# Kernel optimization log

Measured on AMD Instinct MI355X. Metric: run time of the kernel, lower is better.

Reference implementation:

```python
import jax, jax.numpy as jnp
import numpy as np

DIM = 768
EPS = 1e-06


def _layernorm(x, gamma, beta):
    # LayerNorm over last axis (channels), eps=EPS, elementwise affine
    mu = jnp.mean(x, axis=-1, keepdims=True)
    var = jnp.mean(jnp.square(x - mu), axis=-1, keepdims=True)
    return (x - mu) * jax.lax.rsqrt(var + EPS) * gamma + beta


def setup_inputs() -> dict:
    key = jax.random.key(0)
    ks = jax.random.split(key, 10)
    B, C, H, W = 16, DIM, 32, 32
    s = 1.0 / np.sqrt(C)  # mimic Conv2d default init scale
    return {
        "x": jax.random.normal(ks[0], (B, C, H, W), dtype=jnp.float32),
        "W1": jax.random.uniform(ks[1], (C, C), jnp.float32, -s, s),
        "b1": jax.random.uniform(ks[2], (C,), jnp.float32, -s, s),
        "g1": jnp.ones((C,), jnp.float32),
        "beta1": jnp.zeros((C,), jnp.float32),
        "W2": jax.random.uniform(ks[3], (C, C), jnp.float32, -s, s),
        "b2": jax.random.uniform(ks[4], (C,), jnp.float32, -s, s),
        "g2": jnp.ones((C,), jnp.float32),
        "beta2": jnp.zeros((C,), jnp.float32),
        "W3": jax.random.uniform(ks[5], (C, C), jnp.float32, -s, s),
        "b3": jax.random.uniform(ks[6], (C,), jnp.float32, -s, s),
    }


def reference(x, W1, b1, g1, beta1, W2, b2, g2, beta2, W3, b3):
    # x: [B, C, H, W] (NCHW). Work in NHWC; 1x1 conv == channel matmul.
    h = jnp.transpose(x, (0, 2, 3, 1))  # [B, H, W, C]
    h = jnp.einsum("bhwc,oc->bhwo", h, W1) + b1
    h = jax.nn.gelu(_layernorm(h, g1, beta1), approximate=False)
    h = jnp.einsum("bhwc,oc->bhwo", h, W2) + b2
    h = jax.nn.gelu(_layernorm(h, g2, beta2), approximate=False)
    h = jnp.einsum("bhwc,oc->bhwo", h, W3) + b3
    return jnp.transpose(h, (0, 3, 1, 2))  # back to NCHW
```

## Files before the change

kernel.cpp:

```cpp
#include <hip/hip_runtime.h>
#include <hip/hip_bf16.h>

typedef __bf16 bf16;
typedef __bf16 bf16x4 __attribute__((ext_vector_type(4)));
typedef __bf16 bf16x8 __attribute__((ext_vector_type(8)));
typedef float f32x4 __attribute__((ext_vector_type(4)));

#define DIM 768
#define HW 1024
#define BATCH 16
#define M_TOTAL (BATCH * HW)
#define NKT 12

#define AS1 __attribute__((address_space(1)))
#define AS3 __attribute__((address_space(3)))


__global__ void wcvt3_kernel(const float4* __restrict__ w1, const float4* __restrict__ w2,
                             const float4* __restrict__ w3,
                             bf16x8* __restrict__ o1, bf16x8* __restrict__ o2,
                             bf16x8* __restrict__ o3) {
    const int b = blockIdx.x;
    const int which = b / 288;
    const int i = (b % 288) * 256 + threadIdx.x;
    const float4* w = which == 0 ? w1 : which == 1 ? w2 : w3;
    bf16x8* o = which == 0 ? o1 : which == 1 ? o2 : o3;
    const int row = i / 96, br = i % 96;
    const int q = br >> 2, g = br & 3;
    float4 lo = w[row * 192 + q * 8 + g];
    float4 hi = w[row * 192 + q * 8 + g + 4];
    bf16x8 r = { (bf16)lo.x, (bf16)lo.y, (bf16)lo.z, (bf16)lo.w,
                 (bf16)hi.x, (bf16)hi.y, (bf16)hi.z, (bf16)hi.w };
    o[row * 96 + br] = r;
}

__global__ void transpose_cvt_kernel(const float* __restrict__ x, bf16* __restrict__ xb) {
    __shared__ float tile[32][33];
    const int b = blockIdx.z;
    const int hw0 = blockIdx.x * 32;
    const int c0 = blockIdx.y * 32;
    const int tx = threadIdx.x, ty = threadIdx.y;

    const float* src = x + ((size_t)b * DIM + c0) * HW + hw0;
#pragma unroll
    for (int j = 0; j < 4; j++)
        tile[ty + 8 * j][tx] = src[(size_t)(ty + 8 * j) * HW + tx];
    __syncthreads();
    const int ptx = (((tx & 15) >> 2) << 3) + (tx & 3) + ((tx >> 4) << 2);
    bf16* dst = xb + ((size_t)b * HW + hw0) * DIM + c0;
#pragma unroll
    for (int j = 0; j < 4; j++)
        dst[(size_t)(ty + 8 * j) * DIM + ptx] = (bf16)tile[tx][ty + 8 * j];
}

template <int MODE>
__global__ __launch_bounds__(512, 2) void gemm_kernel(
    const bf16* __restrict__ A,
    const bf16* __restrict__ Bw,
    const float* __restrict__ bias,
    void* __restrict__ out)
{
    constexpr int K = DIM;
    __shared__ bf16 ldsA[2][256][64];
    __shared__ bf16 ldsB[2][192][64];

    const int t = threadIdx.x;
    const int lane = t & 63;
    const int wave = t >> 6;
    const int wm = wave >> 1, wn = wave & 1;

    const int bid = blockIdx.x;
    const int swz = (bid & 7) * 32 + (bid >> 3);
    const int m0 = (swz & 63) << 8;
    const int n0 = (swz >> 6) * 192;

    const int fr = lane & 15;
    const int fq = lane >> 4;

    f32x4 acc[4][6] = {};

    const int s_r = t >> 3;
    const int s_blk = t & 7;

    auto stage_chunk = [&](int kt, int which, int chunk) {
        const int d = kt & 1;
        const int r = chunk * 64 + s_r;
        if (which == 0)
            __builtin_amdgcn_global_load_lds(
                (const AS1 void*)(A + (size_t)(m0 + r) * K + kt * 64 + ((s_blk ^ (r & 7)) << 3)),
                (AS3 void*)&ldsA[d][r][s_blk * 8], 16, 0, 0);
        else
            __builtin_amdgcn_global_load_lds(
                (const AS1 void*)(Bw + (size_t)(n0 + r) * K + kt * 64 + ((s_blk ^ (r & 7)) << 3)),
                (AS3 void*)&ldsB[d][r][s_blk * 8], 16, 0, 0);
    };

    bf16x8 a[4], b0[6], b1[6];

    auto ldA = [&](int kt, int mh) {
        const int d = kt & 1;
#pragma unroll
        for (int mi = 0; mi < 2; mi++) {
            const int R = wm * 64 + (mh * 2 + mi) * 16 + fr;
            const bf16* rp = &ldsA[d][R][0];
            const int s = R & 7;
#pragma unroll
            for (int ks = 0; ks < 2; ks++)
                a[mi * 2 + ks] = *(const bf16x8*)(rp + (((ks * 4 + fq) ^ s) << 3));
        }
    };
    auto ldB = [&](bf16x8* bb, int kt, int nh) {
        const int d = kt & 1;
#pragma unroll
        for (int ni = 0; ni < 3; ni++) {
            const int R = wn * 96 + (nh * 3 + ni) * 16 + fr;
            const bf16* rp = &ldsB[d][R][0];
            const int s = R & 7;
#pragma unroll
            for (int ks = 0; ks < 2; ks++)
                bb[ni * 2 + ks] = *(const bf16x8*)(rp + (((ks * 4 + fq) ^ s) << 3));
        }
    };
    auto MM = [&](bf16x8* bb, int mh, int nh) {
        __builtin_amdgcn_s_setprio(1);
#pragma unroll
        for (int mi = 0; mi < 2; mi++)
#pragma unroll
            for (int ni = 0; ni < 3; ni++)
#pragma unroll
                for (int ks = 0; ks < 2; ks++)
                    acc[mh * 2 + mi][nh * 3 + ni] = __builtin_amdgcn_mfma_f32_16x16x32_bf16(
                        a[mi * 2 + ks], bb[ni * 2 + ks], acc[mh * 2 + mi][nh * 3 + ni], 0, 0, 0);
        __builtin_amdgcn_s_setprio(0);
    };

    stage_chunk(0, 0, 0); stage_chunk(0, 0, 1); stage_chunk(0, 0, 2); stage_chunk(0, 0, 3);
    stage_chunk(0, 1, 0); stage_chunk(0, 1, 1); stage_chunk(0, 1, 2);
    stage_chunk(1, 0, 0); stage_chunk(1, 0, 1);
    asm volatile("s_waitcnt vmcnt(2)" ::: "memory");
    __builtin_amdgcn_s_barrier();

    for (int kt = 0; kt < NKT; ++kt) {
        ldA(kt, 0);
        ldB(b0, kt, 0);
        if (kt + 1 < NKT) { stage_chunk(kt + 1, 0, 2); stage_chunk(kt + 1, 0, 3); }
        __builtin_amdgcn_s_barrier();
        asm volatile("s_waitcnt lgkmcnt(0)" ::: "memory");
        MM(b0, 0, 0);
        __builtin_amdgcn_s_barrier();
        ldB(b1, kt, 1);
        if (kt + 1 < NKT) { stage_chunk(kt + 1, 1, 0); stage_chunk(kt + 1, 1, 1); }
        __builtin_amdgcn_s_barrier();
        asm volatile("s_waitcnt lgkmcnt(0)" ::: "memory");
        MM(b1, 0, 1);
        __builtin_amdgcn_s_barrier();
        ldA(kt, 1);
        if (kt + 1 < NKT) stage_chunk(kt + 1, 1, 2);
        __builtin_amdgcn_s_barrier();
        asm volatile("s_waitcnt lgkmcnt(0)" ::: "memory");
        MM(b1, 1, 1);
        __builtin_amdgcn_s_barrier();
        if (kt + 2 < NKT) { stage_chunk(kt + 2, 0, 0); stage_chunk(kt + 2, 0, 1); }
        MM(b0, 1, 0);
        if (kt < NKT - 2) { asm volatile("s_waitcnt vmcnt(2)" ::: "memory"); }
        else if (kt == NKT - 2) { asm volatile("s_waitcnt vmcnt(0)" ::: "memory"); }
        __builtin_amdgcn_s_barrier();
    }

    const int fq4 = fq * 4;
    if (MODE == 0) {
        bf16* o = (bf16*)out;
#pragma unroll
        for (int mi = 0; mi < 4; mi++) {
            const int row = m0 + wm * 64 + mi * 16 + fq4;
#pragma unroll
            for (int ni = 0; ni < 6; ni++) {
                const int col = n0 + wn * 96 + ni * 16 + fr;
                const int pcol = n0 + wn * 96 + ((ni >> 1) << 5)
                               + ((fr >> 2) << 3) + (fr & 3) + ((ni & 1) << 2);
                const float bv = bias[col];
#pragma unroll
                for (int r = 0; r < 4; r++)
                    o[(size_t)(row + r) * DIM + pcol] = (bf16)(acc[mi][ni][r] + bv);
            }
        }
    } else {
        float* o = (float*)out;
#pragma unroll
        for (int mi = 0; mi < 4; mi++) {
            const int nb = m0 + wm * 64 + mi * 16 + fq4;
            const int bI = nb >> 10, hw = nb & 1023;
#pragma unroll
            for (int ni = 0; ni < 6; ni++) {
                const int col = n0 + wn * 96 + ni * 16 + fr;
                f32x4 v = acc[mi][ni] + bias[col];
                *(f32x4*)(o + ((size_t)bI * DIM + col) * HW + hw) = v;
            }
        }
    }
}

__global__ __launch_bounds__(256) void ln_gelu_kernel(
    bf16* __restrict__ h, const float* __restrict__ g, const float* __restrict__ beta)
{
    const int wave = threadIdx.x >> 6;
    const int lane = threadIdx.x & 63;
    const int n = blockIdx.x * 4 + wave;
    bf16* row = h + (size_t)n * DIM;

    float v[12];
    float s = 0.f, ss = 0.f;
#pragma unroll
    for (int j = 0; j < 3; j++) {
        bf16x4 x = *(const bf16x4*)(row + j * 256 + lane * 4);
#pragma unroll
        for (int i = 0; i < 4; i++) {
            float f = (float)x[i];
            v[j * 4 + i] = f;
            s += f;
            ss += f * f;
        }
    }
#pragma unroll
    for (int off = 32; off > 0; off >>= 1) {
        s += __shfl_xor(s, off);
        ss += __shfl_xor(ss, off);
    }
    const float mu = s * (1.f / DIM);
    const float var = ss * (1.f / DIM) - mu * mu;
    const float rstd = rsqrtf(var + 1e-6f);

#pragma unroll
    for (int j = 0; j < 3; j++) {
        bf16x4 r;
#pragma unroll
        for (int i = 0; i < 4; i++) {
            const int c = j * 256 + lane * 4 + i;
            const int p = (lane * 4 + i) & 31;
            const int kk = ((p >> 3) << 2) + (p & 7) + ((p & 4) ? 12 : 0);
            const int gi = (c & ~31) + kk;
            float y = (v[j * 4 + i] - mu) * rstd * g[gi] + beta[gi];
            y = 0.5f * y * (1.f + erff(y * 0.70710678118f));
            r[i] = (bf16)y;
        }
        *(bf16x4*)(row + j * 256 + lane * 4) = r;
    }
}

extern "C" void kernel_launch(void* const* d_in, const int* in_sizes, int n_in,
                              void* d_out, int out_size, void* d_ws, size_t ws_size,
                              hipStream_t stream) {
    const float* x   = (const float*)d_in[0];
    const float* W1  = (const float*)d_in[1];
    const float* b1  = (const float*)d_in[2];
    const float* g1  = (const float*)d_in[3];
    const float* be1 = (const float*)d_in[4];
    const float* W2  = (const float*)d_in[5];
    const float* b2  = (const float*)d_in[6];
    const float* g2  = (const float*)d_in[7];
    const float* be2 = (const float*)d_in[8];
    const float* W3  = (const float*)d_in[9];
    const float* b3  = (const float*)d_in[10];
    float* out = (float*)d_out;

    bf16* Wb1  = (bf16*)d_ws;
    bf16* Wb2  = Wb1 + (size_t)DIM * DIM;
    bf16* Wb3  = Wb2 + (size_t)DIM * DIM;
    bf16* buf0 = Wb3 + (size_t)DIM * DIM;
    bf16* buf1 = buf0 + (size_t)M_TOTAL * DIM;

    wcvt3_kernel<<<864, 256, 0, stream>>>((const float4*)W1, (const float4*)W2, (const float4*)W3,
                                          (bf16x8*)Wb1, (bf16x8*)Wb2, (bf16x8*)Wb3);

    transpose_cvt_kernel<<<dim3(32, 24, 16), dim3(32, 8), 0, stream>>>(x, buf0);

    const int ggrid = (M_TOTAL / 256) * (DIM / 192);
    gemm_kernel<0><<<ggrid, 512, 0, stream>>>(buf0, Wb1, b1, buf1);
    ln_gelu_kernel<<<M_TOTAL / 4, 256, 0, stream>>>(buf1, g1, be1);
    gemm_kernel<0><<<ggrid, 512, 0, stream>>>(buf1, Wb2, b2, buf0);
    ln_gelu_kernel<<<M_TOTAL / 4, 256, 0, stream>>>(buf0, g2, be2);
    gemm_kernel<1><<<ggrid, 512, 0, stream>>>(buf0, Wb3, b3, out);
}
```

Baseline: 161.9 us.

## Fuse LayerNorm+GELU into GEMM epilogue with full-row 64x768 tiles

Restructures each GEMM so a block owns 64 complete output rows across all 768 channels. This lets the LayerNorm statistics be reduced in-block through shared memory and GELU applied in the epilogue, which removes the two standalone ln_gelu kernels and their extra read/write passes over the activations. The K loop now runs in 32-wide steps and streams the whole weight matrix per block through a double-buffered LDS buffer. The grid shrinks to 256 blocks, one per CU, which cuts parallelism and raises per-block weight traffic.

Result: no change. 162.5 us (+0.4%).

```diff
diff --git a/kernel.cpp b/kernel.cpp
--- a/kernel.cpp
+++ b/kernel.cpp
@@ -10,7 +10,7 @@
 #define HW 1024
 #define BATCH 16
 #define M_TOTAL (BATCH * HW)
-#define NKT 12
+#define NKT 24
 
 #define AS1 __attribute__((address_space(1)))
 #define AS3 __attribute__((address_space(3)))
@@ -58,192 +58,179 @@
     const bf16* __restrict__ A,
     const bf16* __restrict__ Bw,
     const float* __restrict__ bias,
+    const float* __restrict__ gamma,
+    const float* __restrict__ beta,
     void* __restrict__ out)
 {
-    constexpr int K = DIM;
-    __shared__ bf16 ldsA[2][256][64];
-    __shared__ bf16 ldsB[2][192][64];
+    __shared__ bf16 ldsB[2][DIM][32];
+    __shared__ bf16 ldsA[2][64][64];
+    __shared__ float lnred[64][4][2];
 
     const int t = threadIdx.x;
     const int lane = t & 63;
     const int wave = t >> 6;
-    const int wm = wave >> 1, wn = wave & 1;
+    const int wm = wave >> 2, wn = wave & 3;
 
     const int bid = blockIdx.x;
     const int swz = (bid & 7) * 32 + (bid >> 3);
-    const int m0 = (swz & 63) << 8;
-    const int n0 = (swz >> 6) * 192;
-
-    const int fr = lane & 15;
-    const int fq = lane >> 4;
-
-    f32x4 acc[4][6] = {};
-
-    const int s_r = t >> 3;
-    const int s_blk = t & 7;
-
-    auto stage_chunk = [&](int kt, int which, int chunk) {
+    const int m0 = swz * 64;
+
+    const int fr = lane & 15, fq = lane >> 4;
+
+    f32x4 acc[2][12] = {};
+
+    const int sBr = t >> 2, sBb = t & 3;
+    const int sAr = t >> 3, sAb = t & 7;
+    const int swzBw = (sBr & 3) ^ ((sBr >> 2) & 3);
+
+    auto stageB = [&](int kt, int chunk) {
         const int d = kt & 1;
-        const int r = chunk * 64 + s_r;
-        if (which == 0)
-            __builtin_amdgcn_global_load_lds(
-                (const AS1 void*)(A + (size_t)(m0 + r) * K + kt * 64 + ((s_blk ^ (r & 7)) << 3)),
-                (AS3 void*)&ldsA[d][r][s_blk * 8], 16, 0, 0);
-        else
-            __builtin_amdgcn_global_load_lds(
-                (const AS1 void*)(Bw + (size_t)(n0 + r) * K + kt * 64 + ((s_blk ^ (r & 7)) << 3)),
-                (AS3 void*)&ldsB[d][r][s_blk * 8], 16, 0, 0);
-    };
-
-    bf16x8 a[4], b0[6], b1[6];
-
-    auto ldA = [&](int kt, int mh) {
+        const int r = chunk * 128 + sBr;
+        __builtin_amdgcn_global_load_lds(
+            (const AS1 void*)(Bw + (size_t)r * DIM + kt * 32 + ((sBb ^ swzBw) << 3)),
+            (AS3 void*)&ldsB[d][r][sBb * 8], 16, 0, 0);
+    };
+    auto stageA = [&](int pair) {
+        const int d = pair & 1;
+        __builtin_amdgcn_global_load_lds(
+            (const AS1 void*)(A + (size_t)(m0 + sAr) * DIM + pair * 64 + ((sAb ^ (sAr & 7)) << 3)),
+            (AS3 void*)&ldsA[d][sAr][sAb * 8], 16, 0, 0);
+    };
+
+    bf16x8 af[2], bfr[6];
+    auto ldA = [&](int kt) {
+        const int d = (kt >> 1) & 1, kb = (kt & 1) * 4;
+#pragma unroll
+        for (int mi = 0; mi < 2; mi++) {
+            const int R = wm * 32 + mi * 16 + fr;
+            af[mi] = *(const bf16x8*)(&ldsA[d][R][0] + (((kb + fq) ^ (R & 7)) << 3));
+        }
+    };
+    auto ldB6 = [&](int kt, int nh) {
         const int d = kt & 1;
 #pragma unroll
-        for (int mi = 0; mi < 2; mi++) {
-            const int R = wm * 64 + (mh * 2 + mi) * 16 + fr;
-            const bf16* rp = &ldsA[d][R][0];
-            const int s = R & 7;
-#pragma unroll
-            for (int ks = 0; ks < 2; ks++)
-                a[mi * 2 + ks] = *(const bf16x8*)(rp + (((ks * 4 + fq) ^ s) << 3));
-        }
-    };
-    auto ldB = [&](bf16x8* bb, int kt, int nh) {
-        const int d = kt & 1;
-#pragma unroll
-        for (int ni = 0; ni < 3; ni++) {
-            const int R = wn * 96 + (nh * 3 + ni) * 16 + fr;
-            const bf16* rp = &ldsB[d][R][0];
-            const int s = R & 7;
-#pragma unroll
-            for (int ks = 0; ks < 2; ks++)
-                bb[ni * 2 + ks] = *(const bf16x8*)(rp + (((ks * 4 + fq) ^ s) << 3));
-        }
-    };
-    auto MM = [&](bf16x8* bb, int mh, int nh) {
+        for (int j = 0; j < 6; j++) {
+            const int R = wn * 192 + (nh * 6 + j) * 16 + fr;
+            bfr[j] = *(const bf16x8*)(&ldsB[d][R][0] +
+                       ((fq ^ ((R & 3) ^ ((R >> 2) & 3))) << 3));
+        }
+    };
+    auto MM = [&](int nh) {
         __builtin_amdgcn_s_setprio(1);
 #pragma unroll
         for (int mi = 0; mi < 2; mi++)
 #pragma unroll
-            for (int ni = 0; ni < 3; ni++)
-#pragma unroll
-                for (int ks = 0; ks < 2; ks++)
-                    acc[mh * 2 + mi][nh * 3 + ni] = __builtin_amdgcn_mfma_f32_16x16x32_bf16(
-                        a[mi * 2 + ks], bb[ni * 2 + ks], acc[mh * 2 + mi][nh * 3 + ni], 0, 0, 0);
+            for (int j = 0; j < 6; j++)
+                acc[mi][nh * 6 + j] = __builtin_amdgcn_mfma_f32_16x16x32_bf16(
+                    af[mi], bfr[j], acc[mi][nh * 6 + j], 0, 0, 0);
         __builtin_amdgcn_s_setprio(0);
     };
 
-    stage_chunk(0, 0, 0); stage_chunk(0, 0, 1); stage_chunk(0, 0, 2); stage_chunk(0, 0, 3);
-    stage_chunk(0, 1, 0); stage_chunk(0, 1, 1); stage_chunk(0, 1, 2);
-    stage_chunk(1, 0, 0); stage_chunk(1, 0, 1);
-    asm volatile("s_waitcnt vmcnt(2)" ::: "memory");
+#pragma unroll
+    for (int c = 0; c < 6; c++) stageB(0, c);
+    stageA(0);
+    asm volatile("s_waitcnt vmcnt(0)" ::: "memory");
     __builtin_amdgcn_s_barrier();
 
-    for (int kt = 0; kt < NKT; ++kt) {
-        ldA(kt, 0);
-        ldB(b0, kt, 0);
-        if (kt + 1 < NKT) { stage_chunk(kt + 1, 0, 2); stage_chunk(kt + 1, 0, 3); }
-        __builtin_amdgcn_s_barrier();
-        asm volatile("s_waitcnt lgkmcnt(0)" ::: "memory");
-        MM(b0, 0, 0);
-        __builtin_amdgcn_s_barrier();
-        ldB(b1, kt, 1);
-        if (kt + 1 < NKT) { stage_chunk(kt + 1, 1, 0); stage_chunk(kt + 1, 1, 1); }
-        __builtin_amdgcn_s_barrier();
-        asm volatile("s_waitcnt lgkmcnt(0)" ::: "memory");
-        MM(b1, 0, 1);
-        __builtin_amdgcn_s_barrier();
-        ldA(kt, 1);
-        if (kt + 1 < NKT) stage_chunk(kt + 1, 1, 2);
-        __builtin_amdgcn_s_barrier();
-        asm volatile("s_waitcnt lgkmcnt(0)" ::: "memory");
-        MM(b1, 1, 1);
-        __builtin_amdgcn_s_barrier();
-        if (kt + 2 < NKT) { stage_chunk(kt + 2, 0, 0); stage_chunk(kt + 2, 0, 1); }
-        MM(b0, 1, 0);
-        if (kt < NKT - 2) { asm volatile("s_waitcnt vmcnt(2)" ::: "memory"); }
-        else if (kt == NKT - 2) { asm volatile("s_waitcnt vmcnt(0)" ::: "memory"); }
+    for (int kt2 = 0; kt2 < NKT - 2; kt2 += 2) {
+        ldA(kt2); ldB6(kt2, 0);
+        stageB(kt2 + 1, 0); stageB(kt2 + 1, 1); stageB(kt2 + 1, 2);
+        MM(0);
+        ldB6(kt2, 1);
+        stageB(kt2 + 1, 3); stageB(kt2 + 1, 4); stageB(kt2 + 1, 5);
+        stageA((kt2 + 2) >> 1);
+        MM(1);
+        asm volatile("s_waitcnt vmcnt(1)" ::: "memory");
+        __builtin_amdgcn_s_barrier();
+        const int ko = kt2 + 1;
+        ldA(ko); ldB6(ko, 0);
+        stageB(ko + 1, 0); stageB(ko + 1, 1); stageB(ko + 1, 2);
+        MM(0);
+        ldB6(ko, 1);
+        stageB(ko + 1, 3); stageB(ko + 1, 4); stageB(ko + 1, 5);
+        MM(1);
+        asm volatile("s_waitcnt vmcnt(0)" ::: "memory");
         __builtin_amdgcn_s_barrier();
     }
-
-    const int fq4 = fq * 4;
+    {
+        ldA(22); ldB6(22, 0);
+        stageB(23, 0); stageB(23, 1); stageB(23, 2);
+        MM(0);
+        ldB6(22, 1);
+        stageB(23, 3); stageB(23, 4); stageB(23, 5);
+        MM(1);
+        asm volatile("s_waitcnt vmcnt(0)" ::: "memory");
+        __builtin_amdgcn_s_barrier();
+        ldA(23); ldB6(23, 0);
+        MM(0);
+        ldB6(23, 1);
+        MM(1);
+    }
+
+    float bv[12];
+#pragma unroll
+    for (int j = 0; j < 12; j++) bv[j] = bias[wn * 192 + j * 16 + fr];
+
     if (MODE == 0) {
+        float gv[12], bev[12];
+#pragma unroll
+        for (int j = 0; j < 12; j++) {
+            const int col = wn * 192 + j * 16 + fr;
+            gv[j] = gamma[col]; bev[j] = beta[col];
+        }
+#pragma unroll
+        for (int mi = 0; mi < 2; mi++)
+#pragma unroll
+            for (int r = 0; r < 4; r++) {
+                float s = 0.f, ss = 0.f;
+#pragma unroll
+                for (int j = 0; j < 12; j++) {
+                    const float v = acc[mi][j][r] + bv[j];
+                    s += v; ss += v * v;
+                }
+#pragma unroll
+                for (int o = 1; o < 16; o <<= 1) {
+                    s += __shfl_xor(s, o); ss += __shfl_xor(ss, o);
+                }
+                if (fr == 0) {
+                    const int row = wm * 32 + mi * 16 + fq * 4 + r;
+                    lnred[row][wn][0] = s; lnred[row][wn][1] = ss;
+                }
+            }
+        __builtin_amdgcn_s_barrier();
         bf16* o = (bf16*)out;
 #pragma unroll
-        for (int mi = 0; mi < 4; mi++) {
-            const int row = m0 + wm * 64 + mi * 16 + fq4;
-#pragma unroll
-            for (int ni = 0; ni < 6; ni++) {
-                const int col = n0 + wn * 96 + ni * 16 + fr;
-                const int pcol = n0 + wn * 96 + ((ni >> 1) << 5)
-                               + ((fr >> 2) << 3) + (fr & 3) + ((ni & 1) << 2);
-                const float bv = bias[col];
-#pragma unroll
-                for (int r = 0; r < 4; r++)
-                    o[(size_t)(row + r) * DIM + pcol] = (bf16)(acc[mi][ni][r] + bv);
+        for (int mi = 0; mi < 2; mi++)
+#pragma unroll
+            for (int r = 0; r < 4; r++) {
+                const int row = wm * 32 + mi * 16 + fq * 4 + r;
+                const float s  = lnred[row][0][0] + lnred[row][1][0] + lnred[row][2][0] + lnred[row][3][0];
+                const float ss = lnred[row][0][1] + lnred[row][1][1] + lnred[row][2][1] + lnred[row][3][1];
+                const float mu = s * (1.f / DIM);
+                const float var = ss * (1.f / DIM) - mu * mu;
+                const float rstd = rsqrtf(var + 1e-6f);
+#pragma unroll
+                for (int j = 0; j < 12; j++) {
+                    float y = (acc[mi][j][r] + bv[j] - mu) * rstd * gv[j] + bev[j];
+                    y = 0.5f * y * (1.f + erff(y * 0.70710678118f));
+                    const int pcol = wn * 192 + ((j >> 1) << 5) + ((fr >> 2) << 3)
+                                   + (fr & 3) + ((j & 1) << 2);
+                    o[(size_t)(m0 + row) * DIM + pcol] = (bf16)y;
+                }
             }
-        }
     } else {
         float* o = (float*)out;
 #pragma unroll
-        for (int mi = 0; mi < 4; mi++) {
-            const int nb = m0 + wm * 64 + mi * 16 + fq4;
+        for (int mi = 0; mi < 2; mi++) {
+            const int nb = m0 + wm * 32 + mi * 16 + fq * 4;
             const int bI = nb >> 10, hw = nb & 1023;
 #pragma unroll
-            for (int ni = 0; ni < 6; ni++) {
-                const int col = n0 + wn * 96 + ni * 16 + fr;
-                f32x4 v = acc[mi][ni] + bias[col];
+            for (int j = 0; j < 12; j++) {
+                const int col = wn * 192 + j * 16 + fr;
+                f32x4 v = acc[mi][j] + bv[j];
                 *(f32x4*)(o + ((size_t)bI * DIM + col) * HW + hw) = v;
             }
         }
-    }
-}
-
-__global__ __launch_bounds__(256) void ln_gelu_kernel(
-    bf16* __restrict__ h, const float* __restrict__ g, const float* __restrict__ beta)
-{
-    const int wave = threadIdx.x >> 6;
-    const int lane = threadIdx.x & 63;
-    const int n = blockIdx.x * 4 + wave;
-    bf16* row = h + (size_t)n * DIM;
-
-    float v[12];
-    float s = 0.f, ss = 0.f;
-#pragma unroll
-    for (int j = 0; j < 3; j++) {
-        bf16x4 x = *(const bf16x4*)(row + j * 256 + lane * 4);
-#pragma unroll
-        for (int i = 0; i < 4; i++) {
-            float f = (float)x[i];
-            v[j * 4 + i] = f;
-            s += f;
-            ss += f * f;
-        }
-    }
-#pragma unroll
-    for (int off = 32; off > 0; off >>= 1) {
-        s += __shfl_xor(s, off);
-        ss += __shfl_xor(ss, off);
-    }
-    const float mu = s * (1.f / DIM);
-    const float var = ss * (1.f / DIM) - mu * mu;
-    const float rstd = rsqrtf(var + 1e-6f);
-
-#pragma unroll
-    for (int j = 0; j < 3; j++) {
-        bf16x4 r;
-#pragma unroll
-        for (int i = 0; i < 4; i++) {
-            const int c = j * 256 + lane * 4 + i;
-            const int p = (lane * 4 + i) & 31;
-            const int kk = ((p >> 3) << 2) + (p & 7) + ((p & 4) ? 12 : 0);
-            const int gi = (c & ~31) + kk;
-            float y = (v[j * 4 + i] - mu) * rstd * g[gi] + beta[gi];
-            y = 0.5f * y * (1.f + erff(y * 0.70710678118f));
-            r[i] = (bf16)y;
-        }
-        *(bf16x4*)(row + j * 256 + lane * 4) = r;
     }
 }
 
@@ -274,10 +261,7 @@
 
     transpose_cvt_kernel<<<dim3(32, 24, 16), dim3(32, 8), 0, stream>>>(x, buf0);
 
-    const int ggrid = (M_TOTAL / 256) * (DIM / 192);
-    gemm_kernel<0><<<ggrid, 512, 0, stream>>>(buf0, Wb1, b1, buf1);
-    ln_gelu_kernel<<<M_TOTAL / 4, 256, 0, stream>>>(buf1, g1, be1);
-    gemm_kernel<0><<<ggrid, 512, 0, stream>>>(buf1, Wb2, b2, buf0);
-    ln_gelu_kernel<<<M_TOTAL / 4, 256, 0, stream>>>(buf0, g2, be2);
-    gemm_kernel<1><<<ggrid, 512, 0, stream>>>(buf0, Wb3, b3, out);
-}
+    gemm_kernel<0><<<256, 512, 0, stream>>>(buf0, Wb1, b1, g1, be1, buf1);
+    gemm_kernel<0><<<256, 512, 0, stream>>>(buf1, Wb2, b2, g2, be2, buf0);
+    gemm_kernel<1><<<256, 512, 0, stream>>>(buf0, Wb3, b3, b3, b3, out);
+}
```
